# Kernel optimization log

Hardware: AMD Instinct MI355X
Metric: run time of the kernel (lower is better)

The kernel has to match this reference:

```python
import jax, jax.numpy as jnp
import numpy as np

B, S, N, BS, D, H, V = 1, 2048, 128, 16, 512, 8, 32000
MASK_TOKEN_ID = 3


def setup_inputs() -> dict:
    key = jax.random.key(0)
    ks = jax.random.split(key, 10)
    anchors = jnp.sort(jax.random.randint(ks[0], (B, N), 0, S - BS), axis=1)
    return {
        "input_ids": jax.random.randint(ks[1], (B, S), 0, V),
        "hidden_states": jax.random.normal(ks[2], (B, S, D), dtype=jnp.float32),
        "loss_mask": jnp.ones((B, S), dtype=jnp.float32),
        "anchor_positions": anchors,
        "block_keep_mask": jnp.ones((B, N), dtype=bool),
        "embed_table": jax.random.normal(ks[3], (V, D), dtype=jnp.float32) * 0.02,
        "Wq": jax.random.normal(ks[4], (D, D), dtype=jnp.float32) * 0.02,
        "Wk": jax.random.normal(ks[5], (D, D), dtype=jnp.float32) * 0.02,
        "Wv": jax.random.normal(ks[6], (D, D), dtype=jnp.float32) * 0.02,
        "Wo": jax.random.normal(ks[7], (D, D), dtype=jnp.float32) * 0.02,
        "W_lm": jax.random.normal(ks[8], (D, V), dtype=jnp.float32) * 0.02,
    }


def dflash_sdpa_mask(anchor_positions, block_keep_mask):
    # KV layout: [context S | block_0 .. block_{N-1}], Q layout: [block_0 .. block_{N-1}]
    Q = N * BS
    KV = S + N * BS
    q_idx = jnp.arange(Q)              # [Q]
    kv_idx = jnp.arange(KV)            # [KV]
    q_blk = q_idx // BS                # [Q]
    anchor_q = anchor_positions[:, q_blk]          # [B,Q] anchor of each query's block
    keep_q = block_keep_mask[:, q_blk]             # [B,Q]
    is_ctx = kv_idx < S                             # [KV]
    mask_context = is_ctx[None, None, :] & (kv_idx[None, None, :] < anchor_q[:, :, None])  # [B,Q,KV]
    kv_blk = (kv_idx - S) // BS
    mask_draft = (kv_idx >= S)[None, :] & (q_blk[:, None] == kv_blk[None, :])              # [Q,KV]
    final = (mask_context | mask_draft[None]) & keep_q[:, :, None]                          # [B,Q,KV]
    return final


def reference(input_ids, hidden_states, loss_mask, anchor_positions, block_keep_mask,
              embed_table, Wq, Wk, Wv, Wo, W_lm):
    dh = D // H
    Q = N * BS

    # --- noise embedding: MASK token everywhere, anchor token at each block start ---
    safe_anchor = jnp.clip(anchor_positions, 0, S - 1)                     # [B,N]
    anchor_tokens = jnp.take_along_axis(input_ids, safe_anchor, axis=1)    # [B,N]
    start_tokens = jnp.where(block_keep_mask, anchor_tokens, MASK_TOKEN_ID)
    noise_ids = jnp.full((B, Q), MASK_TOKEN_ID, dtype=input_ids.dtype)
    noise_ids = noise_ids.at[:, jnp.arange(N) * BS].set(start_tokens)
    noise_embedding = embed_table[noise_ids]                               # [B,Q,D]

    # --- draft attention: Q = draft tokens, KV = [context hiddens | draft tokens] ---
    kv_in = jnp.concatenate([hidden_states, noise_embedding], axis=1)      # [B,S+Q,D]
    q = (noise_embedding @ Wq).reshape(B, Q, H, dh)
    k = (kv_in @ Wk).reshape(B, S + Q, H, dh)
    v = (kv_in @ Wv).reshape(B, S + Q, H, dh)
    scores = jnp.einsum("bqhd,bkhd->bhqk", q, k) / jnp.sqrt(jnp.float32(dh))
    mask = dflash_sdpa_mask(anchor_positions, block_keep_mask)[:, None]    # [B,1,Q,KV]
    attn = jax.nn.softmax(jnp.where(mask, scores, -1e9), axis=-1)
    out = jnp.einsum("bhqk,bkhd->bqhd", attn, v).reshape(B, Q, D) @ Wo     # [B,Q,D]
    logits = out @ W_lm                                                    # [B,Q,V]

    # --- block-wise CE loss ---
    offs = jnp.arange(BS)
    label_idx = anchor_positions[:, :, None] + offs[None, None, :]         # [B,N,BS]
    valid_label = label_idx < S
    safe_idx = jnp.clip(label_idx, 0, S - 1)
    ids_b = jnp.broadcast_to(input_ids[:, None, :], (B, N, S))
    target_ids = jnp.take_along_axis(ids_b, safe_idx, axis=2)              # [B,N,BS]
    lm_b = jnp.broadcast_to(loss_mask[:, None, :], (B, N, S))
    lm_g = jnp.take_along_axis(lm_b, safe_idx, axis=2)
    weight = (block_keep_mask[:, :, None].astype(jnp.float32)
              * valid_label.astype(jnp.float32)
              * (offs > 0)[None, None, :].astype(jnp.float32)
              * lm_g)                                                      # [B,N,BS]

    flat_logits = logits.reshape(-1, V)
    flat_targets = target_ids.reshape(-1)
    flat_w = weight.reshape(-1)
    logp = jax.nn.log_softmax(flat_logits, axis=-1)
    loss_per = -jnp.take_along_axis(logp, flat_targets[:, None], axis=1)[:, 0]
    loss = jnp.sum(loss_per * flat_w) / (jnp.sum(flat_w) + 1e-6)

    pred = jnp.argmax(flat_logits, axis=-1)
    correct = (pred == flat_targets) & (flat_w > 0.5)
    accuracy = jnp.sum(correct).astype(jnp.float32) / (jnp.sum(flat_w) + 1e-6)
    return loss, accuracy
```

## Files before the change

### kernel.cpp

```cpp
#include <hip/hip_runtime.h>

typedef unsigned short u16;
typedef __attribute__((ext_vector_type(4))) float f32x4;
typedef __attribute__((ext_vector_type(8))) short short8;
typedef __attribute__((ext_vector_type(4))) unsigned int uv4;
typedef __attribute__((ext_vector_type(4))) float fv4;
typedef __attribute__((ext_vector_type(4))) unsigned short usv4;

#define S_LEN 2048
#define NBLK 128
#define DMODEL 512
#define VOCAB 32000
#define QLEN 2048
#define KVLEN 4096
#define NSPLIT 250

#define GAS(p) ((const __attribute__((address_space(1))) void*)(const void*)(p))
#define LAS(p) ((__attribute__((address_space(3))) void*)(void*)(p))

__device__ __forceinline__ float bf2f(u16 u){
  union { unsigned int i; float f; } x; x.i = ((unsigned int)u) << 16; return x.f;
}
__device__ __forceinline__ u16 f2bf(float f){
  union { float f; unsigned int i; } x; x.f = f;
  unsigned int r = x.i + 0x7fffu + ((x.i >> 16) & 1u);
  return (u16)(r >> 16);
}

__global__ __launch_bounds__(256) void transpose4(const float* __restrict__ i0, const float* __restrict__ i1,
                                                  const float* __restrict__ i2, const float* __restrict__ i3,
                                                  u16* __restrict__ o0, u16* __restrict__ o1,
                                                  u16* __restrict__ o2, u16* __restrict__ o3){
  const float* in; u16* out;
  switch (blockIdx.z){
    case 0: in = i0; out = o0; break;
    case 1: in = i1; out = o1; break;
    case 2: in = i2; out = o2; break;
    default: in = i3; out = o3; break;
  }
  __shared__ float tile[32][33];
  int t = threadIdx.x, tx = t & 31, ty = t >> 5;
  int nb = blockIdx.x * 32, kb = blockIdx.y * 32;
  #pragma unroll
  for (int i = 0; i < 4; i++){
    int r = ty + i * 8;
    tile[r][tx] = in[(size_t)(kb + r) * 512 + nb + tx];
  }
  __syncthreads();
  #pragma unroll
  for (int i = 0; i < 4; i++){
    int r = ty + i * 8;
    out[(size_t)(nb + r) * 512 + kb + tx] = f2bf(tile[tx][r]);
  }
}

__global__ __launch_bounds__(256) void transpose_cast(const float* __restrict__ in,
                                                      u16* __restrict__ out,
                                                      int K, int N){
  __shared__ float tile[32][33];
  int t = threadIdx.x, tx = t & 31, ty = t >> 5;
  int nb = blockIdx.x * 32, kb = blockIdx.y * 32;
  #pragma unroll
  for (int i = 0; i < 4; i++){
    int r = ty + i * 8;
    tile[r][tx] = in[(size_t)(kb + r) * N + nb + tx];
  }
  __syncthreads();
  #pragma unroll
  for (int i = 0; i < 4; i++){
    int r = ty + i * 8;
    out[(size_t)(nb + r) * K + kb + tx] = f2bf(tile[tx][r]);
  }
}

__global__ __launch_bounds__(128) void build_kv(const float* __restrict__ hidden,
                                                const float* __restrict__ embed,
                                                const int* __restrict__ input_ids,
                                                const int* __restrict__ anchors,
                                                const unsigned char* __restrict__ keep,
                                                u16* __restrict__ kvb){
  int row = blockIdx.x;
  int t = threadIdx.x;
  const float* src;
  if (row < S_LEN){
    src = hidden + (size_t)row * DMODEL;
  } else {
    int q = row - S_LEN;
    int id = 3;
    if ((q & 15) == 0){
      int n = q >> 4;
      if (keep[n]){
        int a = anchors[n]; a = min(max(a, 0), S_LEN - 1);
        id = input_ids[a];
      }
    }
    src = embed + (size_t)id * DMODEL;
  }
  int c = t * 4;
  fv4 v = *(const fv4*)&src[c];
  usv4 o; o[0] = f2bf(v[0]); o[1] = f2bf(v[1]); o[2] = f2bf(v[2]); o[3] = f2bf(v[3]);
  *(usv4*)&kvb[(size_t)row * DMODEL + c] = o;
}

template<int TRANS, int MF>
__global__ __launch_bounds__(256) void gemmTile(const u16* __restrict__ A,
                                                const u16* __restrict__ BT,
                                                u16* __restrict__ C,
                                                int M, int N, int K, int ldc){
  __shared__ __align__(16) u16 As[2][64 * MF * 64];
  __shared__ __align__(16) u16 Bs[2][64 * 64];
  int t = threadIdx.x, w = t >> 6, lane = t & 63;
  int g = lane >> 4, li = lane & 15;
  int rowbase = blockIdx.x * (64 * MF), colbase = blockIdx.y * 64;
  int r0 = t >> 3, cg0 = t & 7;
  int swz = (cg0 ^ (r0 & 7)) << 3;

  auto stageA = [&](u16* dst, int kb){
    #pragma unroll
    for (int i = 0; i < 2 * MF; i++)
      __builtin_amdgcn_global_load_lds(GAS(&A[(size_t)(rowbase + r0 + i * 32) * K + kb + swz]),
                                       LAS(dst + i * 2048 + w * 512), 16, 0, 0);
  };
  auto stageB = [&](u16* dst, int kb){
    #pragma unroll
    for (int i = 0; i < 2; i++)
      __builtin_amdgcn_global_load_lds(GAS(&BT[(size_t)(colbase + r0 + i * 32) * K + kb + swz]),
                                       LAS(dst + i * 2048 + w * 512), 16, 0, 0);
  };

  f32x4 acc[MF][4];
  #pragma unroll
  for (int i = 0; i < MF; i++)
    #pragma unroll
    for (int j = 0; j < 4; j++)
      acc[i][j] = (f32x4){0.f, 0.f, 0.f, 0.f};

  stageA(As[0], 0); stageB(Bs[0], 0);

  int nkt = K >> 6;
  for (int kt = 0; kt < nkt; kt++){
    u16* curA = As[kt & 1]; u16* curB = Bs[kt & 1];
    if (kt + 1 < nkt){
      stageA(As[(kt + 1) & 1], (kt + 1) * 64); stageB(Bs[(kt + 1) & 1], (kt + 1) * 64);
      if constexpr (MF == 2) asm volatile("s_waitcnt vmcnt(6)" ::: "memory");
      else                   asm volatile("s_waitcnt vmcnt(4)" ::: "memory");
    } else {
      asm volatile("s_waitcnt vmcnt(0)" ::: "memory");
    }
    __builtin_amdgcn_s_barrier();
    #pragma unroll
    for (int ks = 0; ks < 2; ks++){
      short8 af[MF], bf[4];
      #pragma unroll
      for (int mf = 0; mf < MF; mf++){
        int row = w * 16 * MF + mf * 16 + li;
        af[mf] = *(const short8*)&curA[row * 64 + (((ks * 4 + g) ^ (li & 7)) << 3)];
      }
      #pragma unroll
      for (int nf = 0; nf < 4; nf++){
        int row = nf * 16 + li;
        bf[nf] = *(const short8*)&curB[row * 64 + (((ks * 4 + g) ^ (li & 7)) << 3)];
      }
      #pragma unroll
      for (int mf = 0; mf < MF; mf++)
        #pragma unroll
        for (int nf = 0; nf < 4; nf++)
          acc[mf][nf] = __builtin_amdgcn_mfma_f32_16x16x32_bf16(af[mf], bf[nf], acc[mf][nf], 0, 0, 0);
    }
    __builtin_amdgcn_s_barrier();
  }

  #pragma unroll
  for (int mf = 0; mf < MF; mf++)
    #pragma unroll
    for (int nf = 0; nf < 4; nf++)
      #pragma unroll
      for (int r = 0; r < 4; r++){
        int row = rowbase + w * 16 * MF + mf * 16 + g * 4 + r;
        int col = colbase + nf * 16 + li;
        u16 vv = f2bf(acc[mf][nf][r]);
        if (TRANS) C[(size_t)col * ldc + row] = vv;
        else       C[(size_t)row * ldc + col] = vv;
      }
}

__global__ __launch_bounds__(256) void attn_mfma(const u16* __restrict__ qb,
                                                 const u16* __restrict__ kb,
                                                 const u16* __restrict__ vT,
                                                 const int* __restrict__ anchors,
                                                 const unsigned char* __restrict__ keep,
                                                 u16* __restrict__ attnb){
  int n = blockIdx.x, h = blockIdx.y;
  int t = threadIdx.x, w = t >> 6, lane = t & 63;
  int g = lane >> 4, li = lane & 15;

  __shared__ __align__(16) u16 q_s[16][72];
  __shared__ __align__(16) u16 p_s[4][16][72];
  __shared__ float o_s[4][16][64];
  __shared__ float ml_s[4][2][16];

  {
    int r = t >> 4, c4 = (t & 15) * 4;
    *(usv4*)&q_s[r][c4] = *(const usv4*)&qb[(size_t)(n * 16 + r) * DMODEL + h * 64 + c4];
  }
  __syncthreads();

  int anchor = anchors[n];
  bool kp = keep[n] != 0;
  const u16* kh  = kb + h * 64;
  const u16* vTh = vT + (size_t)(h * 64) * KVLEN;

  if (!kp){
    if (w == 0){
      float acc = 0.f;
      const u16* row = vTh + (size_t)lane * KVLEN;
      for (int k2 = 0; k2 < KVLEN; k2 += 8){
        short8 vv = *(const short8*)&row[k2];
        #pragma unroll
        for (int j = 0; j < 8; j++) acc += bf2f((u16)vv[j]);
      }
      acc *= (1.f / 4096.f);
      u16 ov = f2bf(acc);
      for (int r = 0; r < 16; r++)
        attnb[(size_t)(n * 16 + r) * DMODEL + h * 64 + lane] = ov;
    }
    return;
  }

  short8 qa[2];
  #pragma unroll
  for (int ks = 0; ks < 2; ks++)
    qa[ks] = *(const short8*)&q_s[li][ks * 32 + g * 8];

  int nctx = (anchor + 63) >> 6;
  int ntot = nctx + 1;

  f32x4 o_acc[4];
  float m[4], l[4];
  #pragma unroll
  for (int i = 0; i < 4; i++){ o_acc[i] = (f32x4){0.f,0.f,0.f,0.f}; m[i] = -3e38f; l[i] = 0.f; }

  for (int c = w; c < ntot; c += 4){
    bool draft = (c == nctx);
    int kbase = draft ? (S_LEN + n * 16) : c * 64;
    int nk    = draft ? 16 : min(64, anchor - c * 64);

    f32x4 s[4];
    #pragma unroll
    for (int nf = 0; nf < 4; nf++) s[nf] = (f32x4){0.f,0.f,0.f,0.f};
    #pragma unroll
    for (int ks = 0; ks < 2; ks++){
      #pragma unroll
      for (int nf = 0; nf < 4; nf++){
        int krow = min(kbase + nf * 16 + li, KVLEN - 1);
        short8 bfrag = *(const short8*)&kh[(size_t)krow * DMODEL + ks * 32 + g * 8];
        s[nf] = __builtin_amdgcn_mfma_f32_16x16x32_bf16(qa[ks], bfrag, s[nf], 0, 0, 0);
      }
    }

    #pragma unroll
    for (int r = 0; r < 4; r++){
      float mx = -3e38f;
      #pragma unroll
      for (int nf = 0; nf < 4; nf++){
        float sv = s[nf][r] * 0.125f;
        if (nf * 16 + li >= nk) sv = -3e38f;
        s[nf][r] = sv;
        mx = fmaxf(mx, sv);
      }
      #pragma unroll
      for (int mm = 1; mm < 16; mm <<= 1) mx = fmaxf(mx, __shfl_xor(mx, mm));
      float mn = fmaxf(m[r], mx);
      float sc = __expf(m[r] - mn);
      float ps = 0.f;
      #pragma unroll
      for (int nf = 0; nf < 4; nf++){
        float p = __expf(s[nf][r] - mn);
        ps += p;
        p_s[w][g * 4 + r][nf * 16 + li] = f2bf(p);
      }
      #pragma unroll
      for (int mm = 1; mm < 16; mm <<= 1) ps += __shfl_xor(ps, mm);
      l[r] = l[r] * sc + ps;
      m[r] = mn;
      #pragma unroll
      for (int nfd = 0; nfd < 4; nfd++) o_acc[nfd][r] *= sc;
    }

    #pragma unroll
    for (int ks = 0; ks < 2; ks++){
      short8 pa = *(const short8*)&p_s[w][li][ks * 32 + g * 8];
      int kcol = min(kbase + ks * 32 + g * 8, KVLEN - 8);
      #pragma unroll
      for (int nfd = 0; nfd < 4; nfd++){
        short8 vfrag = *(const short8*)&vTh[(size_t)(nfd * 16 + li) * KVLEN + kcol];
        o_acc[nfd] = __builtin_amdgcn_mfma_f32_16x16x32_bf16(pa, vfrag, o_acc[nfd], 0, 0, 0);
      }
    }
  }

  #pragma unroll
  for (int r = 0; r < 4; r++){
    if (li == 0){ ml_s[w][0][g * 4 + r] = m[r]; ml_s[w][1][g * 4 + r] = l[r]; }
    #pragma unroll
    for (int nfd = 0; nfd < 4; nfd++)
      o_s[w][g * 4 + r][nfd * 16 + li] = o_acc[nfd][r];
  }
  __syncthreads();

  {
    int row = t >> 4, c0 = (t & 15) * 4;
    float M = -3e38f;
    #pragma unroll
    for (int ww = 0; ww < 4; ww++) M = fmaxf(M, ml_s[ww][0][row]);
    float L = 0.f, ew[4];
    #pragma unroll
    for (int ww = 0; ww < 4; ww++){
      ew[ww] = __expf(ml_s[ww][0][row] - M);
      L += ml_s[ww][1][row] * ew[ww];
    }
    float inv = 1.f / L;
    #pragma unroll
    for (int j = 0; j < 4; j++){
      float ov = 0.f;
      #pragma unroll
      for (int ww = 0; ww < 4; ww++) ov += o_s[ww][row][c0 + j] * ew[ww];
      attnb[(size_t)(n * 16 + row) * DMODEL + h * 64 + c0 + j] = f2bf(ov * inv);
    }
  }
}

__global__ __launch_bounds__(256) void lm_fused(const u16* __restrict__ obp,
                                                const u16* __restrict__ WT,
                                                const int* __restrict__ input_ids,
                                                const int* __restrict__ anchors,
                                                float* __restrict__ pl,
                                                float* __restrict__ pt, float* __restrict__ pbv,
                                                int* __restrict__ pbi){
  __shared__ __align__(16) u16 Wb[2][128 * 32];
  __shared__ __align__(16) u16 Ob[2][128 * 32];
  __shared__ int tcol_s[128];

  int L = blockIdx.x;
  int T = (L & 7) * 500 + (L >> 3);
  int qbase = (T & 15) * 128;
  int vb = T >> 4;
  int vocabbase = vb * 128;
  int t = threadIdx.x, w = t >> 6, lane = t & 63;
  int g = lane >> 4, li = lane & 15;

  if (t < 128){
    int r = qbase + t; int n = r >> 4, off = r & 15;
    int lab = anchors[n] + off;
    int safe = min(max(lab, 0), S_LEN - 1);
    tcol_s[t] = input_ids[safe];
  }

  int sr = t >> 2;
  int scg = (t & 3) ^ ((sr >> 1) & 3);
  auto stage = [&](u16* wdst, u16* odst, int kb){
    #pragma unroll
    for (int i = 0; i < 2; i++){
      __builtin_amdgcn_global_load_lds(GAS(&WT [(size_t)(vocabbase + i * 64 + sr) * DMODEL + kb + (scg << 3)]),
                                       LAS(wdst + i * 2048 + w * 512), 16, 0, 0);
      __builtin_amdgcn_global_load_lds(GAS(&obp[(size_t)(qbase     + i * 64 + sr) * DMODEL + kb + (scg << 3)]),
                                       LAS(odst + i * 2048 + w * 512), 16, 0, 0);
    }
  };

  f32x4 acc[2][8];
  #pragma unroll
  for (int i = 0; i < 2; i++)
    #pragma unroll
    for (int j = 0; j < 8; j++)
      acc[i][j] = (f32x4){0.f, 0.f, 0.f, 0.f};

  stage(Wb[0], Ob[0], 0);

  int cgr = (g ^ ((li >> 1) & 3)) << 3;
  for (int kt = 0; kt < 16; kt++){
    const u16* curW = Wb[kt & 1]; const u16* curO = Ob[kt & 1];
    if (kt < 15){
      stage(Wb[(kt + 1) & 1], Ob[(kt + 1) & 1], (kt + 1) * 32);
      asm volatile("s_waitcnt vmcnt(4)" ::: "memory");
    } else {
      asm volatile("s_waitcnt vmcnt(0)" ::: "memory");
    }
    __builtin_amdgcn_s_barrier();
    __builtin_amdgcn_s_setprio(1);
    short8 wfr[2], obf[8];
    #pragma unroll
    for (int vf = 0; vf < 2; vf++)
      wfr[vf] = *(const short8*)&curW[(w * 32 + vf * 16 + li) * 32 + cgr];
    #pragma unroll
    for (int qf = 0; qf < 8; qf++)
      obf[qf] = *(const short8*)&curO[(qf * 16 + li) * 32 + cgr];
    #pragma unroll
    for (int vf = 0; vf < 2; vf++)
      #pragma unroll
      for (int qf = 0; qf < 8; qf++)
        acc[vf][qf] = __builtin_amdgcn_mfma_f32_16x16x32_bf16(wfr[vf], obf[qf], acc[vf][qf], 0, 0, 0);
    __builtin_amdgcn_s_setprio(0);
    __builtin_amdgcn_s_barrier();
  }
  __syncthreads();

  u16* sb = &Wb[0][0];
  float* cse = (float*)(sb);
  float* ctv = (float*)(sb + 1024);
  float* cbv = (float*)(sb + 2048);
  int*   cbi = (int*)  (sb + 3072);

  #pragma unroll
  for (int qf = 0; qf < 8; qf++){
    int qloc = qf * 16 + li;
    int tc = tcol_s[qloc] - vocabbase;
    float se = 0.f, tv = -3e38f, bv = -3e38f; int bi = 0x7fffffff;
    #pragma unroll
    for (int vf = 0; vf < 2; vf++){
      #pragma unroll
      for (int r = 0; r < 4; r++){
        float v = acc[vf][qf][r];
        int pos = w * 32 + vf * 16 + g * 4 + r;
        se += __expf(v);
        if (pos == tc) tv = v;
        if (v > bv){ bv = v; bi = pos; }
      }
    }
    #pragma unroll
    for (int off = 16; off <= 32; off <<= 1){
      se += __shfl_xor(se, off);
      tv = fmaxf(tv, __shfl_xor(tv, off));
      float ob_ = __shfl_xor(bv, off); int oi = __shfl_xor(bi, off);
      if (ob_ > bv || (ob_ == bv && oi < bi)){ bv = ob_; bi = oi; }
    }
    if (g == 0){
      cse[w * 128 + qloc] = se; ctv[w * 128 + qloc] = tv;
      cbv[w * 128 + qloc] = bv; cbi[w * 128 + qloc] = bi;
    }
  }
  __syncthreads();

  if (t < 128){
    float SE = 0.f, TV = -3e38f, BV = -3e38f; int BI = 0x7fffffff;
    #pragma unroll
    for (int ww = 0; ww < 4; ww++){
      SE += cse[ww * 128 + t];
      TV = fmaxf(TV, ctv[ww * 128 + t]);
      float v = cbv[ww * 128 + t];
      if (v > BV){ BV = v; BI = cbi[ww * 128 + t]; }
    }
    size_t idx = (size_t)vb * QLEN + qbase + t;
    pl[idx] = SE; pt[idx] = TV; pbv[idx] = BV; pbi[idx] = vocabbase + BI;
  }
}

__global__ __launch_bounds__(256) void loss_rows(const float* __restrict__ pl,
                                                 const float* __restrict__ pt, const float* __restrict__ pbv,
                                                 const int* __restrict__ pbi,
                                                 const int* __restrict__ input_ids,
                                                 const int* __restrict__ anchors,
                                                 const unsigned char* __restrict__ keep,
                                                 const float* __restrict__ loss_mask,
                                                 float* __restrict__ rowacc){
  int t = threadIdx.x, w = t >> 6, lane = t & 63;
  int row = blockIdx.x * 4 + w;
  float L = 0.f, TV = -3e38f, BV = -3e38f; int BI = 0x7fffffff;
  for (int s = lane; s < NSPLIT; s += 64){
    size_t idx = (size_t)s * QLEN + row;
    L += pl[idx];
    TV = fmaxf(TV, pt[idx]);
    float bv_ = pbv[idx]; int bi_ = pbi[idx];
    if (bv_ > BV || (bv_ == BV && bi_ < BI)){ BV = bv_; BI = bi_; }
  }
  #pragma unroll
  for (int mm = 1; mm < 64; mm <<= 1){
    L += __shfl_xor(L, mm);
    TV = fmaxf(TV, __shfl_xor(TV, mm));
    float ob = __shfl_xor(BV, mm); int oi = __shfl_xor(BI, mm);
    if (ob > BV || (ob == BV && oi < BI)){ BV = ob; BI = oi; }
  }
  if (lane == 0){
    int n = row >> 4, off = row & 15;
    int lab = anchors[n] + off;
    int valid = (lab < S_LEN) ? 1 : 0;
    int safe = min(max(lab, 0), S_LEN - 1);
    int tgt = input_ids[safe];
    float wgt = (keep[n] ? 1.f : 0.f) * (valid ? 1.f : 0.f) * ((off > 0) ? 1.f : 0.f) * loss_mask[safe];
    float logp = TV - __logf(L);
    rowacc[row * 3 + 0] = -logp * wgt;
    rowacc[row * 3 + 1] = wgt;
    rowacc[row * 3 + 2] = ((BI == tgt) && (wgt > 0.5f)) ? 1.f : 0.f;
  }
}

__global__ __launch_bounds__(256) void final_sum(const float* __restrict__ rowacc, float* __restrict__ out){
  int t = threadIdx.x;
  float a = 0.f, b = 0.f, c = 0.f;
  for (int r = t; r < QLEN; r += 256){
    a += rowacc[r * 3 + 0]; b += rowacc[r * 3 + 1]; c += rowacc[r * 3 + 2];
  }
  __shared__ float sa[256], sb[256], sc_[256];
  sa[t] = a; sb[t] = b; sc_[t] = c;
  __syncthreads();
  for (int s = 128; s >= 1; s >>= 1){
    if (t < s){ sa[t] += sa[t + s]; sb[t] += sb[t + s]; sc_[t] += sc_[t + s]; }
    __syncthreads();
  }
  if (t == 0){
    out[0] = sa[0] / (sb[0] + 1e-6f);
    out[1] = sc_[0] / (sb[0] + 1e-6f);
  }
}

extern "C" void kernel_launch(void* const* d_in, const int* in_sizes, int n_in,
                              void* d_out, int out_size, void* d_ws, size_t ws_size,
                              hipStream_t stream) {
  const int*   input_ids = (const int*)  d_in[0];
  const float* hidden    = (const float*)d_in[1];
  const float* loss_mask = (const float*)d_in[2];
  const int*   anchors   = (const int*)  d_in[3];
  const unsigned char* keep = (const unsigned char*)d_in[4];
  const float* embed     = (const float*)d_in[5];
  const float* Wq        = (const float*)d_in[6];
  const float* Wk        = (const float*)d_in[7];
  const float* Wv        = (const float*)d_in[8];
  const float* Wo        = (const float*)d_in[9];
  const float* Wlm       = (const float*)d_in[10];

  char* ws = (char*)d_ws;
  size_t off = 0;
  auto take = [&](size_t bytes) -> char* {
    char* p = ws + off;
    off += (bytes + 255) & ~(size_t)255;
    return p;
  };
  u16* WqT  = (u16*)take((size_t)512 * 512 * 2);
  u16* WkT  = (u16*)take((size_t)512 * 512 * 2);
  u16* WvT  = (u16*)take((size_t)512 * 512 * 2);
  u16* WoT  = (u16*)take((size_t)512 * 512 * 2);
  u16* WlmT = (u16*)take((size_t)VOCAB * 512 * 2);
  u16* kvb  = (u16*)take((size_t)KVLEN * 512 * 2);
  u16* qb2  = (u16*)take((size_t)QLEN * 512 * 2);
  u16* kb   = (u16*)take((size_t)KVLEN * 512 * 2);
  u16* vTb  = (u16*)take((size_t)512 * KVLEN * 2);
  u16* attnb= (u16*)take((size_t)QLEN * 512 * 2);
  u16* ob   = (u16*)take((size_t)QLEN * 512 * 2);
  float* pl = (float*)take((size_t)QLEN * NSPLIT * 4);
  float* pt = (float*)take((size_t)QLEN * NSPLIT * 4);
  float* pbv= (float*)take((size_t)QLEN * NSPLIT * 4);
  int*   pbi= (int*)  take((size_t)QLEN * NSPLIT * 4);
  float* rowacc = (float*)take((size_t)QLEN * 3 * 4);

  transpose4<<<dim3(16, 16, 4), 256, 0, stream>>>(Wq, Wk, Wv, Wo, WqT, WkT, WvT, WoT);
  transpose_cast<<<dim3(1000, 16), 256, 0, stream>>>(Wlm, WlmT, 512, VOCAB);

  build_kv<<<KVLEN, 128, 0, stream>>>(hidden, embed, input_ids, anchors, keep, kvb);

  gemmTile<0, 2><<<dim3(32, 8), 256, 0, stream>>>(kvb, WkT, kb,  KVLEN, 512, 512, 512);
  gemmTile<1, 2><<<dim3(32, 8), 256, 0, stream>>>(kvb, WvT, vTb, KVLEN, 512, 512, KVLEN);
  gemmTile<0, 1><<<dim3(32, 8), 256, 0, stream>>>(kvb + (size_t)S_LEN * 512, WqT, qb2, QLEN, 512, 512, 512);

  attn_mfma<<<dim3(NBLK, 8), 256, 0, stream>>>(qb2, kb, vTb, anchors, keep, attnb);

  gemmTile<0, 1><<<dim3(32, 8), 256, 0, stream>>>(attnb, WoT, ob, QLEN, 512, 512, 512);

  lm_fused<<<4000, 256, 0, stream>>>(ob, WlmT, input_ids, anchors, pl, pt, pbv, pbi);

  loss_rows<<<512, 256, 0, stream>>>(pl, pt, pbv, pbi, input_ids, anchors, keep, loss_mask, rowacc);

  final_sum<<<1, 256, 0, stream>>>(rowacc, (float*)d_out);
}
```

Before: 244.1 us.

## Pre-swizzle LM head weights into MFMA fragment layout and widen vocab tile

The W_lm transpose now writes bf16 weights directly in per-lane MFMA fragment order, so lm_fused loads W fragments straight from global memory into registers instead of staging them through LDS. The vocab tile per block doubles to 256 (64 per wave), halving the grid and the number of partial reductions (NSPLIT 125), and the k-loop is unrolled by two with ping-pong register buffers for W. This cuts LDS traffic and re-reads of the activation tile, at the cost of more accumulator and W registers per thread, which may lower occupancy.

```diff
diff --git a/kernel.cpp b/kernel.cpp
--- a/kernel.cpp
+++ b/kernel.cpp
@@ -13,7 +13,7 @@
 #define VOCAB 32000
 #define QLEN 2048
 #define KVLEN 4096
-#define NSPLIT 250
+#define NSPLIT 125
 
 #define GAS(p) ((const __attribute__((address_space(1))) void*)(const void*)(p))
 #define LAS(p) ((__attribute__((address_space(3))) void*)(void*)(p))
@@ -54,23 +54,26 @@
   }
 }
 
-__global__ __launch_bounds__(256) void transpose_cast(const float* __restrict__ in,
-                                                      u16* __restrict__ out,
-                                                      int K, int N){
+__global__ __launch_bounds__(256) void transpose_wlm_frag(const float* __restrict__ in,
+                                                          u16* __restrict__ Wf){
   __shared__ float tile[32][33];
   int t = threadIdx.x, tx = t & 31, ty = t >> 5;
-  int nb = blockIdx.x * 32, kb = blockIdx.y * 32;
+  int vb32 = blockIdx.x, kt = blockIdx.y;
   #pragma unroll
   for (int i = 0; i < 4; i++){
     int r = ty + i * 8;
-    tile[r][tx] = in[(size_t)(kb + r) * N + nb + tx];
-  }
-  __syncthreads();
-  #pragma unroll
-  for (int i = 0; i < 4; i++){
-    int r = ty + i * 8;
-    out[(size_t)(nb + r) * K + kb + tx] = f2bf(tile[tx][r]);
-  }
+    tile[r][tx] = in[(size_t)(kt * 32 + r) * VOCAB + vb32 * 32 + tx];
+  }
+  __syncthreads();
+  int v_local = t >> 3, gg = t & 7;
+  int g = gg >> 1, j0 = (gg & 1) * 4;
+  int v = vb32 * 32 + v_local;
+  int v16 = v >> 4, li = v & 15;
+  usv4 o;
+  #pragma unroll
+  for (int jj = 0; jj < 4; jj++)
+    o[jj] = f2bf(tile[g * 8 + j0 + jj][v_local]);
+  *(usv4*)&Wf[(size_t)(((v16 * 16 + kt) * 64) + g * 16 + li) * 8 + j0] = o;
 }
 
 __global__ __launch_bounds__(128) void build_kv(const float* __restrict__ hidden,
@@ -331,21 +334,20 @@
 }
 
 __global__ __launch_bounds__(256) void lm_fused(const u16* __restrict__ obp,
-                                                const u16* __restrict__ WT,
+                                                const u16* __restrict__ Wf,
                                                 const int* __restrict__ input_ids,
                                                 const int* __restrict__ anchors,
                                                 float* __restrict__ pl,
                                                 float* __restrict__ pt, float* __restrict__ pbv,
                                                 int* __restrict__ pbi){
-  __shared__ __align__(16) u16 Wb[2][128 * 32];
   __shared__ __align__(16) u16 Ob[2][128 * 32];
   __shared__ int tcol_s[128];
 
   int L = blockIdx.x;
-  int T = (L & 7) * 500 + (L >> 3);
+  int T = (L & 7) * 250 + (L >> 3);
   int qbase = (T & 15) * 128;
   int vb = T >> 4;
-  int vocabbase = vb * 128;
+  int vocabbase = vb * 256;
   int t = threadIdx.x, w = t >> 6, lane = t & 63;
   int g = lane >> 4, li = lane & 15;
 
@@ -358,70 +360,76 @@
 
   int sr = t >> 2;
   int scg = (t & 3) ^ ((sr >> 1) & 3);
-  auto stage = [&](u16* wdst, u16* odst, int kb){
-    #pragma unroll
-    for (int i = 0; i < 2; i++){
-      __builtin_amdgcn_global_load_lds(GAS(&WT [(size_t)(vocabbase + i * 64 + sr) * DMODEL + kb + (scg << 3)]),
-                                       LAS(wdst + i * 2048 + w * 512), 16, 0, 0);
-      __builtin_amdgcn_global_load_lds(GAS(&obp[(size_t)(qbase     + i * 64 + sr) * DMODEL + kb + (scg << 3)]),
+  auto stageO = [&](u16* odst, int kt){
+    #pragma unroll
+    for (int i = 0; i < 2; i++)
+      __builtin_amdgcn_global_load_lds(GAS(&obp[(size_t)(qbase + i * 64 + sr) * DMODEL + kt * 32 + (scg << 3)]),
                                        LAS(odst + i * 2048 + w * 512), 16, 0, 0);
-    }
   };
-
-  f32x4 acc[2][8];
-  #pragma unroll
-  for (int i = 0; i < 2; i++)
+  const u16* wbase = Wf + ((size_t)(vb * 16 + w * 4) * 16) * 512 + lane * 8;
+  auto loadW = [&](short8 (&wreg)[4], int kt){
+    #pragma unroll
+    for (int vf = 0; vf < 4; vf++)
+      wreg[vf] = *(const short8*)(wbase + ((size_t)(vf * 16 + kt) * 64) * 8);
+  };
+
+  f32x4 acc[4][8];
+  #pragma unroll
+  for (int i = 0; i < 4; i++)
     #pragma unroll
     for (int j = 0; j < 8; j++)
       acc[i][j] = (f32x4){0.f, 0.f, 0.f, 0.f};
 
-  stage(Wb[0], Ob[0], 0);
+  short8 wA[4], wB[4];
+  stageO(Ob[0], 0);
+  loadW(wA, 0);
 
   int cgr = (g ^ ((li >> 1) & 3)) << 3;
-  for (int kt = 0; kt < 16; kt++){
-    const u16* curW = Wb[kt & 1]; const u16* curO = Ob[kt & 1];
+  auto body = [&](int kt, const u16* curO, u16* nxtO, short8 (&wcur)[4], short8 (&wnext)[4]){
     if (kt < 15){
-      stage(Wb[(kt + 1) & 1], Ob[(kt + 1) & 1], (kt + 1) * 32);
-      asm volatile("s_waitcnt vmcnt(4)" ::: "memory");
+      stageO(nxtO, kt + 1);
+      loadW(wnext, kt + 1);
+      asm volatile("s_waitcnt vmcnt(6)" ::: "memory");
     } else {
       asm volatile("s_waitcnt vmcnt(0)" ::: "memory");
     }
     __builtin_amdgcn_s_barrier();
     __builtin_amdgcn_s_setprio(1);
-    short8 wfr[2], obf[8];
-    #pragma unroll
-    for (int vf = 0; vf < 2; vf++)
-      wfr[vf] = *(const short8*)&curW[(w * 32 + vf * 16 + li) * 32 + cgr];
+    short8 obf[8];
     #pragma unroll
     for (int qf = 0; qf < 8; qf++)
       obf[qf] = *(const short8*)&curO[(qf * 16 + li) * 32 + cgr];
     #pragma unroll
-    for (int vf = 0; vf < 2; vf++)
+    for (int vf = 0; vf < 4; vf++)
       #pragma unroll
       for (int qf = 0; qf < 8; qf++)
-        acc[vf][qf] = __builtin_amdgcn_mfma_f32_16x16x32_bf16(wfr[vf], obf[qf], acc[vf][qf], 0, 0, 0);
+        acc[vf][qf] = __builtin_amdgcn_mfma_f32_16x16x32_bf16(wcur[vf], obf[qf], acc[vf][qf], 0, 0, 0);
     __builtin_amdgcn_s_setprio(0);
     __builtin_amdgcn_s_barrier();
-  }
-  __syncthreads();
-
-  u16* sb = &Wb[0][0];
-  float* cse = (float*)(sb);
-  float* ctv = (float*)(sb + 1024);
-  float* cbv = (float*)(sb + 2048);
-  int*   cbi = (int*)  (sb + 3072);
+  };
+
+  for (int kt = 0; kt < 16; kt += 2){
+    body(kt,     Ob[0], Ob[1], wA, wB);
+    body(kt + 1, Ob[1], Ob[0], wB, wA);
+  }
+  __syncthreads();
+
+  float* cse = (float*)&Ob[0][0];
+  float* ctv = (float*)&Ob[0][2048];
+  float* cbv = (float*)&Ob[1][0];
+  int*   cbi = (int*)  &Ob[1][2048];
 
   #pragma unroll
   for (int qf = 0; qf < 8; qf++){
     int qloc = qf * 16 + li;
-    int tc = tcol_s[qloc] - vocabbase;
+    int tc = tcol_s[qloc] - (vocabbase + w * 64);
     float se = 0.f, tv = -3e38f, bv = -3e38f; int bi = 0x7fffffff;
     #pragma unroll
-    for (int vf = 0; vf < 2; vf++){
+    for (int vf = 0; vf < 4; vf++){
       #pragma unroll
       for (int r = 0; r < 4; r++){
         float v = acc[vf][qf][r];
-        int pos = w * 32 + vf * 16 + g * 4 + r;
+        int pos = vf * 16 + g * 4 + r;
         se += __expf(v);
         if (pos == tc) tv = v;
         if (v > bv){ bv = v; bi = pos; }
@@ -436,7 +444,7 @@
     }
     if (g == 0){
       cse[w * 128 + qloc] = se; ctv[w * 128 + qloc] = tv;
-      cbv[w * 128 + qloc] = bv; cbi[w * 128 + qloc] = bi;
+      cbv[w * 128 + qloc] = bv; cbi[w * 128 + qloc] = bi + w * 64;
     }
   }
   __syncthreads();
@@ -539,7 +547,7 @@
   u16* WkT  = (u16*)take((size_t)512 * 512 * 2);
   u16* WvT  = (u16*)take((size_t)512 * 512 * 2);
   u16* WoT  = (u16*)take((size_t)512 * 512 * 2);
-  u16* WlmT = (u16*)take((size_t)VOCAB * 512 * 2);
+  u16* Wfrag= (u16*)take((size_t)VOCAB * 512 * 2);
   u16* kvb  = (u16*)take((size_t)KVLEN * 512 * 2);
   u16* qb2  = (u16*)take((size_t)QLEN * 512 * 2);
   u16* kb   = (u16*)take((size_t)KVLEN * 512 * 2);
@@ -553,7 +561,7 @@
   float* rowacc = (float*)take((size_t)QLEN * 3 * 4);
 
   transpose4<<<dim3(16, 16, 4), 256, 0, stream>>>(Wq, Wk, Wv, Wo, WqT, WkT, WvT, WoT);
-  transpose_cast<<<dim3(1000, 16), 256, 0, stream>>>(Wlm, WlmT, 512, VOCAB);
+  transpose_wlm_frag<<<dim3(1000, 16), 256, 0, stream>>>(Wlm, Wfrag);
 
   build_kv<<<KVLEN, 128, 0, stream>>>(hidden, embed, input_ids, anchors, keep, kvb);
 
@@ -565,7 +573,7 @@
 
   gemmTile<0, 1><<<dim3(32, 8), 256, 0, stream>>>(attnb, WoT, ob, QLEN, 512, 512, 512);
 
-  lm_fused<<<4000, 256, 0, stream>>>(ob, WlmT, input_ids, anchors, pl, pt, pbv, pbi);
+  lm_fused<<<2000, 256, 0, stream>>>(ob, Wfrag, input_ids, anchors, pl, pt, pbv, pbi);
 
   loss_rows<<<512, 256, 0, stream>>>(pl, pt, pbv, pbi, input_ids, anchors, keep, loss_mask, rowacc);
 
```

After: 289.8 us. +18.7%, slower.
